# Kernel optimization log

Hardware: AMD Instinct MI355X
Metric: run time of the kernel (lower is better)

## Reference

```python
import jax, jax.numpy as jnp
import numpy as np

N = 50000      # nodes
E = 800000     # edges
IN = 128       # in_channels
HID = 32       # hidden_channels (per head)
HEADS = 4
OUT = 128      # out_channels
NEG_SLOPE = 0.2  # PyG GATConv leaky relu slope


def setup_inputs() -> dict:
    key = jax.random.key(0)
    ks = jax.random.split(key, 10)
    x = jax.random.normal(ks[0], (N, IN), dtype=jnp.float32)
    edge_index = jax.random.randint(ks[1], (2, E), 0, N, dtype=jnp.int32)
    s1 = 1.0 / np.sqrt(IN)
    s2 = 1.0 / np.sqrt(HEADS * HID)
    W1 = jax.random.normal(ks[2], (IN, HEADS * HID), dtype=jnp.float32) * s1
    a_src1 = jax.random.normal(ks[3], (HEADS, HID), dtype=jnp.float32) * s1
    a_dst1 = jax.random.normal(ks[4], (HEADS, HID), dtype=jnp.float32) * s1
    b1 = jnp.zeros((HEADS * HID,), dtype=jnp.float32)
    W2 = jax.random.normal(ks[5], (HEADS * HID, OUT), dtype=jnp.float32) * s2
    a_src2 = jax.random.normal(ks[6], (1, OUT), dtype=jnp.float32) * s2
    a_dst2 = jax.random.normal(ks[7], (1, OUT), dtype=jnp.float32) * s2
    b2 = jnp.zeros((OUT,), dtype=jnp.float32)
    return {"x": x, "edge_index": edge_index, "W1": W1, "a_src1": a_src1,
            "a_dst1": a_dst1, "b1": b1, "W2": W2, "a_src2": a_src2,
            "a_dst2": a_dst2, "b2": b2}


def _gat_layer(x, src, dst, W, a_src, a_dst, bias, heads, out_c, concat, n):
    # dense projection then reshape to [N, H, C]
    h = (x @ W).reshape(n, heads, out_c)
    # per-node attention halves: [N, H]
    alpha_src = jnp.einsum('nhc,hc->nh', h, a_src)
    alpha_dst = jnp.einsum('nhc,hc->nh', h, a_dst)
    # per-edge logits, leaky relu (slope 0.2 as in PyG)
    logits = jax.nn.leaky_relu(alpha_src[src] + alpha_dst[dst], NEG_SLOPE)  # [E', H]
    # segment softmax over incoming edges of each destination node
    m = jax.ops.segment_max(logits, dst, num_segments=n)          # [N, H]
    e = jnp.exp(logits - m[dst])                                   # [E', H]
    denom = jax.ops.segment_sum(e, dst, num_segments=n)           # [N, H]
    alpha = e / (denom[dst] + 1e-16)                               # [E', H]
    # weighted scatter-aggregate of source features
    out = jax.ops.segment_sum(alpha[:, :, None] * h[src], dst, num_segments=n)  # [N, H, C]
    if concat:
        out = out.reshape(n, heads * out_c)
    else:
        out = out.mean(axis=1)
    return out + bias


def reference(x, edge_index, W1, a_src1, a_dst1, b1, W2, a_src2, a_dst2, b2):
    n = x.shape[0]
    # PyG GATConv adds self-loops by default
    loop = jnp.arange(n, dtype=edge_index.dtype)
    src = jnp.concatenate([edge_index[0], loop])
    dst = jnp.concatenate([edge_index[1], loop])
    h = _gat_layer(x, src, dst, W1, a_src1, a_dst1, b1, HEADS, HID, True, n)
    h = jax.nn.elu(h)
    # dropout is identity in eval mode
    out = _gat_layer(h, src, dst, W2, a_src2, a_dst2, b2, 1, OUT, False, n)
    return jax.nn.elu(out)
```

## Files before the change

### kernel.cpp

```cpp
#include <hip/hip_runtime.h>
#include <hip/hip_bf16.h>


typedef _Float16 half2_t __attribute__((ext_vector_type(2)));
typedef _Float16 half4_t __attribute__((ext_vector_type(4)));
typedef _Float16 f16x8 __attribute__((ext_vector_type(8)));
typedef float f32x4 __attribute__((ext_vector_type(4)));

static __device__ __forceinline__ float leaky02(float x) {
    return x > 0.f ? x : 0.2f * x;
}
static __device__ __forceinline__ float elu1(float x) {
    return x > 0.f ? x : __expf(x) - 1.f;
}


__global__ void init_prep_kernel(int* __restrict__ cnt, int n,
                                 const float* __restrict__ W1,
                                 const float* __restrict__ W2,
                                 _Float16* __restrict__ Wt1,
                                 _Float16* __restrict__ Wt2, int nInit) {
    int b = blockIdx.x;
    int t = threadIdx.x;
    if (b < nInit) {
        int i = b * 256 + t;
        if (i < n) cnt[i] = 1;
    } else {
        int idx = (b - nInit) * 256 + t;
        int which = idx >> 14;
        int r = idx & 16383;
        int nc = r >> 7, k = r & 127;
        if (which == 0)
            Wt1[(size_t)nc * 128 + k] = (_Float16)W1[(size_t)k * 128 + nc];
        else
            Wt2[(size_t)nc * 128 + k] = (_Float16)W2[(size_t)k * 128 + nc];
    }
}


__global__ void hist_x_kernel(const int* __restrict__ dst, int* __restrict__ cnt,
                              int e, int n, int nch) {
    int b = blockIdx.x;
    int range = b & 7, chunk = b >> 3;
    int rsz = (n + 7) >> 3;
    int rlo = range * rsz;
    int rhi = min(n, rlo + rsz);
    int csz = (e + nch - 1) / nch;
    int lo = chunk * csz;
    int hi = min(e, lo + csz);
    for (int i = lo + (int)threadIdx.x; i < hi; i += 256) {
        int d = dst[i];
        if (d >= rlo && d < rhi) atomicAdd(&cnt[d], 1);
    }
}

__global__ void scan_tile_kernel(const int* __restrict__ in, int* __restrict__ out,
                                 int* __restrict__ sums, int n) {
    __shared__ int sdata[256];
    int t = threadIdx.x;
    int base = blockIdx.x * 2048 + t * 8;
    int v[8];
    int run = 0;
#pragma unroll
    for (int i = 0; i < 8; ++i) {
        int idx = base + i;
        int x = (idx < n) ? in[idx] : 0;
        run += x;
        v[i] = run;
    }
    sdata[t] = run;
    __syncthreads();
    for (int off = 1; off < 256; off <<= 1) {
        int u = (t >= off) ? sdata[t - off] : 0;
        __syncthreads();
        sdata[t] += u;
        __syncthreads();
    }
    int excl = sdata[t] - run;
#pragma unroll
    for (int i = 0; i < 8; ++i) {
        int idx = base + i;
        if (idx < n) out[idx] = v[i] + excl;
    }
    if (t == 0) sums[blockIdx.x] = sdata[255];
}

__global__ void scan_sums_kernel(int* __restrict__ sums, int nb) {
    int t = threadIdx.x;
    int orig = (t < nb) ? sums[t] : 0;
    int v = orig;
#pragma unroll
    for (int off = 1; off < 64; off <<= 1) {
        int u = __shfl_up(v, off, 64);
        if (t >= off) v += u;
    }
    if (t < nb) sums[t] = v - orig;
}

__global__ void scan_finish_kernel(const int* __restrict__ incl, const int* __restrict__ sums,
                                   int* __restrict__ row_ptr, int* __restrict__ cursor, int n) {
    int i = blockIdx.x * blockDim.x + threadIdx.x;
    if (i < n) {
        row_ptr[i + 1] = incl[i] + sums[i >> 11];
        cursor[i] = (i == 0) ? 0 : incl[i - 1] + sums[(i - 1) >> 11];
    }
    if (i == 0) row_ptr[0] = 0;
}


__global__ __launch_bounds__(256) void gemm1_fused_kernel(
    const float* __restrict__ X, const _Float16* __restrict__ Wt,
    _Float16* __restrict__ H16, int nrows, const int* __restrict__ src,
    const int* __restrict__ dst, int* __restrict__ cursor, int* __restrict__ csr,
    int E, int nGemm, int nScatCh) {
    int b = blockIdx.x;
    int t = threadIdx.x;
    if (b < nGemm) {
        int wave = t >> 6, lane = t & 63;
        int m = lane & 15, q = lane >> 4;
        int arow = b * 64 + wave * 16 + m;
        bool rowok = arow < nrows;
        const float* xr = X + (size_t)arow * 128;
        f16x8 afrag[4];
#pragma unroll
        for (int s = 0; s < 4; ++s) {
            float4 v0 = make_float4(0.f, 0.f, 0.f, 0.f);
            float4 v1 = make_float4(0.f, 0.f, 0.f, 0.f);
            if (rowok) {
                v0 = *(const float4*)(xr + s * 32 + q * 8);
                v1 = *(const float4*)(xr + s * 32 + q * 8 + 4);
            }
            f16x8 a;
            a[0] = (_Float16)v0.x; a[1] = (_Float16)v0.y;
            a[2] = (_Float16)v0.z; a[3] = (_Float16)v0.w;
            a[4] = (_Float16)v1.x; a[5] = (_Float16)v1.y;
            a[6] = (_Float16)v1.z; a[7] = (_Float16)v1.w;
            afrag[s] = a;
        }
#pragma unroll
        for (int c = 0; c < 8; ++c) {
            f32x4 acc = {0.f, 0.f, 0.f, 0.f};
#pragma unroll
            for (int s = 0; s < 4; ++s) {
                f16x8 bfrag = *(const f16x8*)(Wt + (size_t)(c * 16 + m) * 128 + s * 32 + q * 8);
                acc = __builtin_amdgcn_mfma_f32_16x16x32_f16(afrag[s], bfrag, acc, 0, 0, 0);
            }
#pragma unroll
            for (int r = 0; r < 4; ++r) {
                int orow = b * 64 + wave * 16 + q * 4 + r;
                if (orow < nrows)
                    H16[(size_t)orow * 128 + c * 16 + m] = (_Float16)acc[r];
            }
        }
    } else {
        int sb = b - nGemm;
        int range = b & 7;
        int chunk = sb >> 3;
        int rsz = (nrows + 7) >> 3;
        int rlo = range * rsz;
        int rhi = min(nrows, rlo + rsz);
        int csz = (E + nScatCh - 1) / nScatCh;
        int lo = chunk * csz;
        int hi = min(E, lo + csz);
        for (int i = lo + t; i < hi; i += 256) {
            int d = dst[i];
            if (d >= rlo && d < rhi) {
                int p = atomicAdd(&cursor[d], 1);
                csr[p] = src[i];
            }
        }
        if (chunk == 0) {
            for (int i = rlo + t; i < rhi; i += 256) {
                int p = atomicAdd(&cursor[i], 1);
                csr[p] = i;
            }
        }
    }
}

__global__ __launch_bounds__(256) void gemm2_mfma_kernel(
    const _Float16* __restrict__ A16, const _Float16* __restrict__ Wt,
    _Float16* __restrict__ H16, int nrows) {
    int b = blockIdx.x;
    int t = threadIdx.x;
    int wave = t >> 6, lane = t & 63;
    int m = lane & 15, q = lane >> 4;
    int arow = b * 64 + wave * 16 + m;
    bool rowok = arow < nrows;
    const _Float16* ar = A16 + (size_t)arow * 128;
    f16x8 afrag[4];
#pragma unroll
    for (int s = 0; s < 4; ++s) {
        f16x8 a = {};
        if (rowok) a = *(const f16x8*)(ar + s * 32 + q * 8);
        afrag[s] = a;
    }
#pragma unroll
    for (int c = 0; c < 8; ++c) {
        f32x4 acc = {0.f, 0.f, 0.f, 0.f};
#pragma unroll
        for (int s = 0; s < 4; ++s) {
            f16x8 bfrag = *(const f16x8*)(Wt + (size_t)(c * 16 + m) * 128 + s * 32 + q * 8);
            acc = __builtin_amdgcn_mfma_f32_16x16x32_f16(afrag[s], bfrag, acc, 0, 0, 0);
        }
#pragma unroll
        for (int r = 0; r < 4; ++r) {
            int orow = b * 64 + wave * 16 + q * 4 + r;
            if (orow < nrows)
                H16[(size_t)orow * 128 + c * 16 + m] = (_Float16)acc[r];
        }
    }
}

__global__ void alpha1_kernel(const _Float16* __restrict__ H16, const float* __restrict__ a_src,
                              const float* __restrict__ a_dst, float* __restrict__ asrc_out,
                              float* __restrict__ adst_out, int n) {
    int wave = (blockIdx.x * blockDim.x + threadIdx.x) >> 6;
    int lane = threadIdx.x & 63;
    if (wave >= n) return;
    int c = lane * 2;
    half2_t hv = *(const half2_t*)(H16 + (size_t)wave * 128 + c);
    float2 as = *(const float2*)(a_src + c);
    float2 ad = *(const float2*)(a_dst + c);
    float hx = (float)hv.x, hy = (float)hv.y;
    float ps = hx * as.x + hy * as.y;
    float pd = hx * ad.x + hy * ad.y;
#pragma unroll
    for (int off = 1; off <= 8; off <<= 1) {
        ps += __shfl_xor(ps, off, 64);
        pd += __shfl_xor(pd, off, 64);
    }
    if ((lane & 15) == 0) {
        int h = lane >> 4;
        asrc_out[wave * 4 + h] = ps;
        adst_out[wave * 4 + h] = pd;
    }
}

__global__ void alpha2_kernel(const _Float16* __restrict__ H16, const float* __restrict__ a_src,
                              const float* __restrict__ a_dst, float* __restrict__ asrc_out,
                              float* __restrict__ adst_out, int n) {
    int wave = (blockIdx.x * blockDim.x + threadIdx.x) >> 6;
    int lane = threadIdx.x & 63;
    if (wave >= n) return;
    int c = lane * 2;
    half2_t hv = *(const half2_t*)(H16 + (size_t)wave * 128 + c);
    float2 as = *(const float2*)(a_src + c);
    float2 ad = *(const float2*)(a_dst + c);
    float hx = (float)hv.x, hy = (float)hv.y;
    float ps = hx * as.x + hy * as.y;
    float pd = hx * ad.x + hy * ad.y;
#pragma unroll
    for (int off = 1; off <= 32; off <<= 1) {
        ps += __shfl_xor(ps, off, 64);
        pd += __shfl_xor(pd, off, 64);
    }
    if (lane == 0) {
        asrc_out[wave] = ps;
        adst_out[wave] = pd;
    }
}


__global__ __launch_bounds__(256) void agg1_kernel(
    const _Float16* __restrict__ H16, const float* __restrict__ asrc,
    const float* __restrict__ adst, const int* __restrict__ row_ptr,
    const int* __restrict__ csr, const float* __restrict__ bias,
    _Float16* __restrict__ out16, int n) {
    int wid = (blockIdx.x * blockDim.x + threadIdx.x) >> 6;
    int lane = threadIdx.x & 63;
    int node = wid * 2 + (lane >> 5);
    if (node >= n) return;
    int sub = lane & 31;
    int c = sub * 4;
    int h = sub >> 3;
    float adh = adst[node * 4 + h];
    float4 bv = *(const float4*)(bias + c);
    int e0 = row_ptr[node];
    int e1 = row_ptr[node + 1];
    float den = 0.f, a0 = 0.f, a1 = 0.f, a2 = 0.f, a3 = 0.f;
    int e = e0;
    for (; e + 4 <= e1; e += 4) {
        int s0 = csr[e + 0], s1 = csr[e + 1], s2 = csr[e + 2], s3 = csr[e + 3];
        float l0 = asrc[s0 * 4 + h];
        float l1 = asrc[s1 * 4 + h];
        float l2 = asrc[s2 * 4 + h];
        float l3 = asrc[s3 * 4 + h];
        half4_t g0 = *(const half4_t*)(H16 + (size_t)s0 * 128 + c);
        half4_t g1 = *(const half4_t*)(H16 + (size_t)s1 * 128 + c);
        half4_t g2 = *(const half4_t*)(H16 + (size_t)s2 * 128 + c);
        half4_t g3 = *(const half4_t*)(H16 + (size_t)s3 * 128 + c);
        float w0 = __expf(leaky02(l0 + adh));
        float w1 = __expf(leaky02(l1 + adh));
        float w2 = __expf(leaky02(l2 + adh));
        float w3 = __expf(leaky02(l3 + adh));
        den += (w0 + w1) + (w2 + w3);
        a0 += w0 * (float)g0.x + w1 * (float)g1.x + w2 * (float)g2.x + w3 * (float)g3.x;
        a1 += w0 * (float)g0.y + w1 * (float)g1.y + w2 * (float)g2.y + w3 * (float)g3.y;
        a2 += w0 * (float)g0.z + w1 * (float)g1.z + w2 * (float)g2.z + w3 * (float)g3.z;
        a3 += w0 * (float)g0.w + w1 * (float)g1.w + w2 * (float)g2.w + w3 * (float)g3.w;
    }
    for (; e < e1; ++e) {
        int s = csr[e];
        float w = __expf(leaky02(asrc[s * 4 + h] + adh));
        half4_t g = *(const half4_t*)(H16 + (size_t)s * 128 + c);
        den += w;
        a0 += w * (float)g.x;
        a1 += w * (float)g.y;
        a2 += w * (float)g.z;
        a3 += w * (float)g.w;
    }
    float inv = 1.f / (den + 1e-16f);
    half4_t o;
    o.x = (_Float16)elu1(a0 * inv + bv.x);
    o.y = (_Float16)elu1(a1 * inv + bv.y);
    o.z = (_Float16)elu1(a2 * inv + bv.z);
    o.w = (_Float16)elu1(a3 * inv + bv.w);
    *(half4_t*)(out16 + (size_t)node * 128 + c) = o;
}

__global__ __launch_bounds__(256) void agg2_kernel(
    const _Float16* __restrict__ H16, const float* __restrict__ asrc,
    const float* __restrict__ adst, const int* __restrict__ row_ptr,
    const int* __restrict__ csr, const float* __restrict__ bias,
    float* __restrict__ out, int n) {
    int wid = (blockIdx.x * blockDim.x + threadIdx.x) >> 6;
    int lane = threadIdx.x & 63;
    int node = wid * 2 + (lane >> 5);
    if (node >= n) return;
    int sub = lane & 31;
    int c = sub * 4;
    float adh = adst[node];
    float4 bv = *(const float4*)(bias + c);
    int e0 = row_ptr[node];
    int e1 = row_ptr[node + 1];
    float den = 0.f, a0 = 0.f, a1 = 0.f, a2 = 0.f, a3 = 0.f;
    int e = e0;
    for (; e + 4 <= e1; e += 4) {
        int s0 = csr[e + 0], s1 = csr[e + 1], s2 = csr[e + 2], s3 = csr[e + 3];
        float l0 = asrc[s0];
        float l1 = asrc[s1];
        float l2 = asrc[s2];
        float l3 = asrc[s3];
        half4_t g0 = *(const half4_t*)(H16 + (size_t)s0 * 128 + c);
        half4_t g1 = *(const half4_t*)(H16 + (size_t)s1 * 128 + c);
        half4_t g2 = *(const half4_t*)(H16 + (size_t)s2 * 128 + c);
        half4_t g3 = *(const half4_t*)(H16 + (size_t)s3 * 128 + c);
        float w0 = __expf(leaky02(l0 + adh));
        float w1 = __expf(leaky02(l1 + adh));
        float w2 = __expf(leaky02(l2 + adh));
        float w3 = __expf(leaky02(l3 + adh));
        den += (w0 + w1) + (w2 + w3);
        a0 += w0 * (float)g0.x + w1 * (float)g1.x + w2 * (float)g2.x + w3 * (float)g3.x;
        a1 += w0 * (float)g0.y + w1 * (float)g1.y + w2 * (float)g2.y + w3 * (float)g3.y;
        a2 += w0 * (float)g0.z + w1 * (float)g1.z + w2 * (float)g2.z + w3 * (float)g3.z;
        a3 += w0 * (float)g0.w + w1 * (float)g1.w + w2 * (float)g2.w + w3 * (float)g3.w;
    }
    for (; e < e1; ++e) {
        int s = csr[e];
        float w = __expf(leaky02(asrc[s] + adh));
        half4_t g = *(const half4_t*)(H16 + (size_t)s * 128 + c);
        den += w;
        a0 += w * (float)g.x;
        a1 += w * (float)g.y;
        a2 += w * (float)g.z;
        a3 += w * (float)g.w;
    }
    float inv = 1.f / (den + 1e-16f);
    float4 o;
    o.x = elu1(a0 * inv + bv.x);
    o.y = elu1(a1 * inv + bv.y);
    o.z = elu1(a2 * inv + bv.z);
    o.w = elu1(a3 * inv + bv.w);
    *(float4*)(out + (size_t)node * 128 + c) = o;
}


extern "C" void kernel_launch(void* const* d_in, const int* in_sizes, int n_in,
                              void* d_out, int out_size, void* d_ws, size_t ws_size,
                              hipStream_t stream) {
    const float* x       = (const float*)d_in[0];
    const int*   eidx    = (const int*)d_in[1];
    const float* W1      = (const float*)d_in[2];
    const float* a_src1  = (const float*)d_in[3];
    const float* a_dst1  = (const float*)d_in[4];
    const float* b1      = (const float*)d_in[5];
    const float* W2      = (const float*)d_in[6];
    const float* a_src2  = (const float*)d_in[7];
    const float* a_dst2  = (const float*)d_in[8];
    const float* b2      = (const float*)d_in[9];
    float* out = (float*)d_out;

    const int N = in_sizes[0] / 128;
    const int E = in_sizes[1] / 2;
    const int* src = eidx;
    const int* dst = eidx + E;

    char* w = (char*)d_ws;
    _Float16* bufH16 = (_Float16*)w; w += (size_t)N * 128 * sizeof(_Float16);
    _Float16* bufA16 = (_Float16*)w; w += (size_t)N * 128 * sizeof(_Float16);
    _Float16* Wt1    = (_Float16*)w; w += (size_t)128 * 128 * sizeof(_Float16);
    _Float16* Wt2    = (_Float16*)w; w += (size_t)128 * 128 * sizeof(_Float16);
    float* asrc = (float*)w;   w += (size_t)N * 4 * sizeof(float);
    float* adst = (float*)w;   w += (size_t)N * 4 * sizeof(float);
    int* cnt     = (int*)w;    w += (size_t)N * sizeof(int);
    int* incl    = (int*)w;    w += (size_t)N * sizeof(int);
    int* row_ptr = (int*)w;    w += (size_t)(N + 1) * sizeof(int);
    int* cursor  = (int*)w;    w += (size_t)N * sizeof(int);
    int* sums    = (int*)w;    w += 64 * sizeof(int);
    int* csr     = (int*)w;    w += (size_t)(E + N) * sizeof(int);

    const int ntiles = (N + 2047) / 2048;
    dim3 b256(256);
    dim3 gN((N + 255) / 256);
    dim3 gWave((N + 3) / 4);
    dim3 gAgg(((((N + 1) / 2) + 3) / 4));
    const int nGemm = (((N + 63) / 64) + 7) & ~7;
    const int nInit = (N + 255) / 256;
    const int histCh = 200;
    const int scatCh = 96;

    hipLaunchKernelGGL(init_prep_kernel, dim3(nInit + 128), b256, 0, stream, cnt, N, W1, W2,
                       Wt1, Wt2, nInit);
    hipLaunchKernelGGL(hist_x_kernel, dim3(8 * histCh), b256, 0, stream, dst, cnt, E, N, histCh);
    hipLaunchKernelGGL(scan_tile_kernel, dim3(ntiles), b256, 0, stream, cnt, incl, sums, N);
    hipLaunchKernelGGL(scan_sums_kernel, dim3(1), dim3(64), 0, stream, sums, ntiles);
    hipLaunchKernelGGL(scan_finish_kernel, gN, b256, 0, stream, incl, sums, row_ptr, cursor, N);

    hipLaunchKernelGGL(gemm1_fused_kernel, dim3(nGemm + 8 * scatCh), b256, 0, stream, x, Wt1,
                       bufH16, N, src, dst, cursor, csr, E, nGemm, scatCh);
    hipLaunchKernelGGL(alpha1_kernel, gWave, b256, 0, stream, bufH16, a_src1, a_dst1, asrc, adst, N);
    hipLaunchKernelGGL(agg1_kernel, gAgg, b256, 0, stream, bufH16, asrc, adst, row_ptr, csr, b1,
                       bufA16, N);

    hipLaunchKernelGGL(gemm2_mfma_kernel, dim3((N + 63) / 64), b256, 0, stream, bufA16, Wt2,
                       bufH16, N);
    hipLaunchKernelGGL(alpha2_kernel, gWave, b256, 0, stream, bufH16, a_src2, a_dst2, asrc, adst, N);
    hipLaunchKernelGGL(agg2_kernel, gAgg, b256, 0, stream, bufH16, asrc, adst, row_ptr, csr, b2,
                       out, N);
}
```

Measured before the change: 296.7 us.

## Build CSR via two-pass bucketed counting sort with shared-memory local sort

```diff
diff --git a/kernel.cpp b/kernel.cpp
--- a/kernel.cpp
+++ b/kernel.cpp
@@ -7,6 +7,9 @@
 typedef _Float16 f16x8 __attribute__((ext_vector_type(8)));
 typedef float f32x4 __attribute__((ext_vector_type(4)));
 
+#define NBLK1 128
+#define SORT_CAP 6144
+
 static __device__ __forceinline__ float leaky02(float x) {
     return x > 0.f ? x : 0.2f * x;
 }
@@ -15,18 +18,22 @@
 }
 
 
-__global__ void init_prep_kernel(int* __restrict__ cnt, int n,
-                                 const float* __restrict__ W1,
-                                 const float* __restrict__ W2,
-                                 _Float16* __restrict__ Wt1,
-                                 _Float16* __restrict__ Wt2, int nInit) {
+__global__ __launch_bounds__(256) void prep_kernel(
+    const int* __restrict__ dst, int* __restrict__ g_cnt, int E, int chunk,
+    const float* __restrict__ W1, const float* __restrict__ W2,
+    _Float16* __restrict__ Wt1, _Float16* __restrict__ Wt2, int nbkt) {
     int b = blockIdx.x;
     int t = threadIdx.x;
-    if (b < nInit) {
-        int i = b * 256 + t;
-        if (i < n) cnt[i] = 1;
+    if (b < NBLK1) {
+        __shared__ int h[256];
+        h[t] = 0;
+        __syncthreads();
+        int lo = b * chunk, hi = min(E, lo + chunk);
+        for (int i = lo + t; i < hi; i += 256) atomicAdd(&h[dst[i] >> 8], 1);
+        __syncthreads();
+        if (t < nbkt) g_cnt[t * NBLK1 + b] = h[t];
     } else {
-        int idx = (b - nInit) * 256 + t;
+        int idx = (b - NBLK1) * 256 + t;
         int which = idx >> 14;
         int r = idx & 16383;
         int nc = r >> 7, k = r & 127;
@@ -37,23 +44,6 @@
     }
 }
 
-
-__global__ void hist_x_kernel(const int* __restrict__ dst, int* __restrict__ cnt,
-                              int e, int n, int nch) {
-    int b = blockIdx.x;
-    int range = b & 7, chunk = b >> 3;
-    int rsz = (n + 7) >> 3;
-    int rlo = range * rsz;
-    int rhi = min(n, rlo + rsz);
-    int csz = (e + nch - 1) / nch;
-    int lo = chunk * csz;
-    int hi = min(e, lo + csz);
-    for (int i = lo + (int)threadIdx.x; i < hi; i += 256) {
-        int d = dst[i];
-        if (d >= rlo && d < rhi) atomicAdd(&cnt[d], 1);
-    }
-}
-
 __global__ void scan_tile_kernel(const int* __restrict__ in, int* __restrict__ out,
                                  int* __restrict__ sums, int n) {
     __shared__ int sdata[256];
@@ -97,22 +87,18 @@
     if (t < nb) sums[t] = v - orig;
 }
 
-__global__ void scan_finish_kernel(const int* __restrict__ incl, const int* __restrict__ sums,
-                                   int* __restrict__ row_ptr, int* __restrict__ cursor, int n) {
+__global__ void offs_kernel(const int* __restrict__ incl, const int* __restrict__ sums,
+                            int* __restrict__ offs, int ncnt) {
     int i = blockIdx.x * blockDim.x + threadIdx.x;
-    if (i < n) {
-        row_ptr[i + 1] = incl[i] + sums[i >> 11];
-        cursor[i] = (i == 0) ? 0 : incl[i - 1] + sums[(i - 1) >> 11];
-    }
-    if (i == 0) row_ptr[0] = 0;
+    if (i <= ncnt) offs[i] = (i == 0) ? 0 : incl[i - 1] + sums[(i - 1) >> 11];
 }
 
 
 __global__ __launch_bounds__(256) void gemm1_fused_kernel(
     const float* __restrict__ X, const _Float16* __restrict__ Wt,
     _Float16* __restrict__ H16, int nrows, const int* __restrict__ src,
-    const int* __restrict__ dst, int* __restrict__ cursor, int* __restrict__ csr,
-    int E, int nGemm, int nScatCh) {
+    const int* __restrict__ dst, const int* __restrict__ offs,
+    int2* __restrict__ binned, int E, int chunk, int nGemm, int nbkt) {
     int b = blockIdx.x;
     int t = threadIdx.x;
     if (b < nGemm) {
@@ -153,27 +139,94 @@
             }
         }
     } else {
+        __shared__ int cur[256];
         int sb = b - nGemm;
-        int range = b & 7;
-        int chunk = sb >> 3;
-        int rsz = (nrows + 7) >> 3;
-        int rlo = range * rsz;
-        int rhi = min(nrows, rlo + rsz);
-        int csz = (E + nScatCh - 1) / nScatCh;
-        int lo = chunk * csz;
-        int hi = min(E, lo + csz);
+        if (t < nbkt) cur[t] = offs[t * NBLK1 + sb];
+        __syncthreads();
+        int lo = sb * chunk, hi = min(E, lo + chunk);
         for (int i = lo + t; i < hi; i += 256) {
             int d = dst[i];
-            if (d >= rlo && d < rhi) {
-                int p = atomicAdd(&cursor[d], 1);
-                csr[p] = src[i];
-            }
-        }
-        if (chunk == 0) {
-            for (int i = rlo + t; i < rhi; i += 256) {
-                int p = atomicAdd(&cursor[i], 1);
-                csr[p] = i;
-            }
+            int s = src[i];
+            int p = atomicAdd(&cur[d >> 8], 1);
+            binned[p] = make_int2(s, d);
+        }
+    }
+}
+
+
+__global__ __launch_bounds__(256) void sort_alpha1_kernel(
+    const int2* __restrict__ binned, const int* __restrict__ offs,
+    int* __restrict__ row_ptr, int* __restrict__ csr, int n, int nbkt,
+    const _Float16* __restrict__ H16, const float* __restrict__ a_src,
+    const float* __restrict__ a_dst, float* __restrict__ asrc_out,
+    float* __restrict__ adst_out) {
+    int b = blockIdx.x;
+    int t = threadIdx.x;
+    if (b < nbkt) {
+        __shared__ int sorted[SORT_CAP];
+        __shared__ int sdata[256];
+        __shared__ int cur[256];
+        int estart = offs[b * NBLK1];
+        int eend = offs[(b + 1) * NBLK1];
+        int node0 = b * 256;
+        int nloc = min(256, n - node0);
+        int cnt0 = (t < nloc) ? 1 : 0;
+        cur[t] = cnt0;
+        __syncthreads();
+        for (int i = estart + t; i < eend; i += 256)
+            atomicAdd(&cur[binned[i].y & 255], 1);
+        __syncthreads();
+        int my = cur[t];
+        sdata[t] = my;
+        __syncthreads();
+        for (int off = 1; off < 256; off <<= 1) {
+            int u = (t >= off) ? sdata[t - off] : 0;
+            __syncthreads();
+            sdata[t] += u;
+            __syncthreads();
+        }
+        int excl = sdata[t] - my;
+        int total = sdata[255];
+        int csr_base = estart + node0;
+        if (node0 + t <= n) row_ptr[node0 + t] = csr_base + excl;
+        if (t == 0 && node0 + 256 <= n) row_ptr[node0 + 256] = csr_base + total;
+        if (t < nloc) {
+            if (excl < SORT_CAP) sorted[excl] = node0 + t;
+            else csr[csr_base + excl] = node0 + t;
+            cur[t] = excl + 1;
+        } else {
+            cur[t] = 0;
+        }
+        __syncthreads();
+        for (int i = estart + t; i < eend; i += 256) {
+            int2 pr = binned[i];
+            int p = atomicAdd(&cur[pr.y & 255], 1);
+            if (p < SORT_CAP) sorted[p] = pr.x;
+            else csr[csr_base + p] = pr.x;
+        }
+        __syncthreads();
+        int lim = min(total, SORT_CAP);
+        for (int j = t; j < lim; j += 256) csr[csr_base + j] = sorted[j];
+    } else {
+        int node = (b - nbkt) * 4 + (t >> 6);
+        int lane = t & 63;
+        if (node >= n) return;
+        int c = lane * 2;
+        half2_t hv = *(const half2_t*)(H16 + (size_t)node * 128 + c);
+        float2 as = *(const float2*)(a_src + c);
+        float2 ad = *(const float2*)(a_dst + c);
+        float hx = (float)hv.x, hy = (float)hv.y;
+        float ps = hx * as.x + hy * as.y;
+        float pd = hx * ad.x + hy * ad.y;
+#pragma unroll
+        for (int off = 1; off <= 8; off <<= 1) {
+            ps += __shfl_xor(ps, off, 64);
+            pd += __shfl_xor(pd, off, 64);
+        }
+        if ((lane & 15) == 0) {
+            int h = lane >> 4;
+            asrc_out[node * 4 + h] = ps;
+            adst_out[node * 4 + h] = pd;
         }
     }
 }
@@ -209,31 +262,6 @@
             if (orow < nrows)
                 H16[(size_t)orow * 128 + c * 16 + m] = (_Float16)acc[r];
         }
-    }
-}
-
-__global__ void alpha1_kernel(const _Float16* __restrict__ H16, const float* __restrict__ a_src,
-                              const float* __restrict__ a_dst, float* __restrict__ asrc_out,
-                              float* __restrict__ adst_out, int n) {
-    int wave = (blockIdx.x * blockDim.x + threadIdx.x) >> 6;
-    int lane = threadIdx.x & 63;
-    if (wave >= n) return;
-    int c = lane * 2;
-    half2_t hv = *(const half2_t*)(H16 + (size_t)wave * 128 + c);
-    float2 as = *(const float2*)(a_src + c);
-    float2 ad = *(const float2*)(a_dst + c);
-    float hx = (float)hv.x, hy = (float)hv.y;
-    float ps = hx * as.x + hy * as.y;
-    float pd = hx * ad.x + hy * ad.y;
-#pragma unroll
-    for (int off = 1; off <= 8; off <<= 1) {
-        ps += __shfl_xor(ps, off, 64);
-        pd += __shfl_xor(pd, off, 64);
-    }
-    if ((lane & 15) == 0) {
-        int h = lane >> 4;
-        asrc_out[wave * 4 + h] = ps;
-        adst_out[wave * 4 + h] = pd;
     }
 }
 
@@ -280,12 +308,31 @@
     int e1 = row_ptr[node + 1];
     float den = 0.f, a0 = 0.f, a1 = 0.f, a2 = 0.f, a3 = 0.f;
     int e = e0;
+    for (; e + 8 <= e1; e += 8) {
+        int s[8];
+#pragma unroll
+        for (int j = 0; j < 8; ++j) s[j] = csr[e + j];
+        float l[8];
+        half4_t g[8];
+#pragma unroll
+        for (int j = 0; j < 8; ++j) {
+            l[j] = asrc[s[j] * 4 + h];
+            g[j] = *(const half4_t*)(H16 + (size_t)s[j] * 128 + c);
+        }
+#pragma unroll
+        for (int j = 0; j < 8; ++j) {
+            float w = __expf(leaky02(l[j] + adh));
+            den += w;
+            a0 += w * (float)g[j].x;
+            a1 += w * (float)g[j].y;
+            a2 += w * (float)g[j].z;
+            a3 += w * (float)g[j].w;
+        }
+    }
     for (; e + 4 <= e1; e += 4) {
         int s0 = csr[e + 0], s1 = csr[e + 1], s2 = csr[e + 2], s3 = csr[e + 3];
-        float l0 = asrc[s0 * 4 + h];
-        float l1 = asrc[s1 * 4 + h];
-        float l2 = asrc[s2 * 4 + h];
-        float l3 = asrc[s3 * 4 + h];
+        float l0 = asrc[s0 * 4 + h], l1 = asrc[s1 * 4 + h];
+        float l2 = asrc[s2 * 4 + h], l3 = asrc[s3 * 4 + h];
         half4_t g0 = *(const half4_t*)(H16 + (size_t)s0 * 128 + c);
         half4_t g1 = *(const half4_t*)(H16 + (size_t)s1 * 128 + c);
         half4_t g2 = *(const half4_t*)(H16 + (size_t)s2 * 128 + c);
@@ -336,12 +383,30 @@
     int e1 = row_ptr[node + 1];
     float den = 0.f, a0 = 0.f, a1 = 0.f, a2 = 0.f, a3 = 0.f;
     int e = e0;
+    for (; e + 8 <= e1; e += 8) {
+        int s[8];
+#pragma unroll
+        for (int j = 0; j < 8; ++j) s[j] = csr[e + j];
+        float l[8];
+        half4_t g[8];
+#pragma unroll
+        for (int j = 0; j < 8; ++j) {
+            l[j] = asrc[s[j]];
+            g[j] = *(const half4_t*)(H16 + (size_t)s[j] * 128 + c);
+        }
+#pragma unroll
+        for (int j = 0; j < 8; ++j) {
+            float w = __expf(leaky02(l[j] + adh));
+            den += w;
+            a0 += w * (float)g[j].x;
+            a1 += w * (float)g[j].y;
+            a2 += w * (float)g[j].z;
+            a3 += w * (float)g[j].w;
+        }
+    }
     for (; e + 4 <= e1; e += 4) {
         int s0 = csr[e + 0], s1 = csr[e + 1], s2 = csr[e + 2], s3 = csr[e + 3];
-        float l0 = asrc[s0];
-        float l1 = asrc[s1];
-        float l2 = asrc[s2];
-        float l3 = asrc[s3];
+        float l0 = asrc[s0], l1 = asrc[s1], l2 = asrc[s2], l3 = asrc[s3];
         half4_t g0 = *(const half4_t*)(H16 + (size_t)s0 * 128 + c);
         half4_t g1 = *(const half4_t*)(H16 + (size_t)s1 * 128 + c);
         half4_t g2 = *(const half4_t*)(H16 + (size_t)s2 * 128 + c);
@@ -396,46 +461,48 @@
     const int* src = eidx;
     const int* dst = eidx + E;
 
+    const int nbkt = (N + 255) >> 8;
+    const int ncnt = nbkt * NBLK1;
+    const int chunk = (E + NBLK1 - 1) / NBLK1;
+    const int ntiles = (ncnt + 2047) / 2048;
+
     char* w = (char*)d_ws;
     _Float16* bufH16 = (_Float16*)w; w += (size_t)N * 128 * sizeof(_Float16);
-    _Float16* bufA16 = (_Float16*)w; w += (size_t)N * 128 * sizeof(_Float16);
     _Float16* Wt1    = (_Float16*)w; w += (size_t)128 * 128 * sizeof(_Float16);
     _Float16* Wt2    = (_Float16*)w; w += (size_t)128 * 128 * sizeof(_Float16);
     float* asrc = (float*)w;   w += (size_t)N * 4 * sizeof(float);
     float* adst = (float*)w;   w += (size_t)N * 4 * sizeof(float);
-    int* cnt     = (int*)w;    w += (size_t)N * sizeof(int);
-    int* incl    = (int*)w;    w += (size_t)N * sizeof(int);
+    int* g_cnt   = (int*)w;    w += (size_t)ncnt * sizeof(int);
+    int* incl    = (int*)w;    w += (size_t)ncnt * sizeof(int);
+    int* offs    = (int*)w;    w += (size_t)(ncnt + 1) * sizeof(int);
+    int* sums    = (int*)w;    w += 64 * sizeof(int);
     int* row_ptr = (int*)w;    w += (size_t)(N + 1) * sizeof(int);
-    int* cursor  = (int*)w;    w += (size_t)N * sizeof(int);
-    int* sums    = (int*)w;    w += 64 * sizeof(int);
+    int2* binned = (int2*)w;   w += (size_t)E * sizeof(int2);
     int* csr     = (int*)w;    w += (size_t)(E + N) * sizeof(int);
-
-    const int ntiles = (N + 2047) / 2048;
+    _Float16* bufA16 = (_Float16*)d_out;
+
     dim3 b256(256);
-    dim3 gN((N + 255) / 256);
-    dim3 gWave((N + 3) / 4);
+    const int nGemm = (N + 63) / 64;
+    const int nAlpha = (N + 3) / 4;
     dim3 gAgg(((((N + 1) / 2) + 3) / 4));
-    const int nGemm = (((N + 63) / 64) + 7) & ~7;
-    const int nInit = (N + 255) / 256;
-    const int histCh = 200;
-    const int scatCh = 96;
-
-    hipLaunchKernelGGL(init_prep_kernel, dim3(nInit + 128), b256, 0, stream, cnt, N, W1, W2,
-                       Wt1, Wt2, nInit);
-    hipLaunchKernelGGL(hist_x_kernel, dim3(8 * histCh), b256, 0, stream, dst, cnt, E, N, histCh);
-    hipLaunchKernelGGL(scan_tile_kernel, dim3(ntiles), b256, 0, stream, cnt, incl, sums, N);
+
+    hipLaunchKernelGGL(prep_kernel, dim3(NBLK1 + 128), b256, 0, stream, dst, g_cnt, E, chunk,
+                       W1, W2, Wt1, Wt2, nbkt);
+    hipLaunchKernelGGL(scan_tile_kernel, dim3(ntiles), b256, 0, stream, g_cnt, incl, sums, ncnt);
     hipLaunchKernelGGL(scan_sums_kernel, dim3(1), dim3(64), 0, stream, sums, ntiles);
-    hipLaunchKernelGGL(scan_finish_kernel, gN, b256, 0, stream, incl, sums, row_ptr, cursor, N);
-
-    hipLaunchKernelGGL(gemm1_fused_kernel, dim3(nGemm + 8 * scatCh), b256, 0, stream, x, Wt1,
-                       bufH16, N, src, dst, cursor, csr, E, nGemm, scatCh);
-    hipLaunchKernelGGL(alpha1_kernel, gWave, b256, 0, stream, bufH16, a_src1, a_dst1, asrc, adst, N);
+    hipLaunchKernelGGL(offs_kernel, dim3((ncnt + 256) / 256 + 1), b256, 0, stream, incl, sums,
+                       offs, ncnt);
+
+    hipLaunchKernelGGL(gemm1_fused_kernel, dim3(nGemm + NBLK1), b256, 0, stream, x, Wt1,
+                       bufH16, N, src, dst, offs, binned, E, chunk, nGemm, nbkt);
+    hipLaunchKernelGGL(sort_alpha1_kernel, dim3(nbkt + nAlpha), b256, 0, stream, binned, offs,
+                       row_ptr, csr, N, nbkt, bufH16, a_src1, a_dst1, asrc, adst);
     hipLaunchKernelGGL(agg1_kernel, gAgg, b256, 0, stream, bufH16, asrc, adst, row_ptr, csr, b1,
                        bufA16, N);
 
-    hipLaunchKernelGGL(gemm2_mfma_kernel, dim3((N + 63) / 64), b256, 0, stream, bufA16, Wt2,
-                       bufH16, N);
-    hipLaunchKernelGGL(alpha2_kernel, gWave, b256, 0, stream, bufH16, a_src2, a_dst2, asrc, adst, N);
+    hipLaunchKernelGGL(gemm2_mfma_kernel, dim3(nGemm), b256, 0, stream, bufA16, Wt2, bufH16, N);
+    hipLaunchKernelGGL(alpha2_kernel, dim3(nAlpha), b256, 0, stream, bufH16, a_src2, a_dst2,
+                       asrc, adst, N);
     hipLaunchKernelGGL(agg2_kernel, gAgg, b256, 0, stream, bufH16, asrc, adst, row_ptr, csr, b2,
                        out, N);
 }
```

New measurement: 247.3 us. -16.7%, faster.
